# Performance work log

Measured on AMD Instinct MI355X. Metric: run time of the kernel, lower is better.

The kernel has to match this reference:

```python
import jax, jax.numpy as jnp
import numpy as np

HEAD_SIZE = 64
EMB_SIZE = 1024
B, N = 4, 4096


def setup_inputs() -> dict:
    key = jax.random.key(0)
    kx, kk, kq, kv = jax.random.split(key, 4)
    x = jax.random.normal(kx, (B, N, EMB_SIZE), dtype=jnp.float32)
    # nn.Linear(emb, head, bias=False): weight [head, emb]; y = x @ W.T
    s = 1.0 / np.sqrt(EMB_SIZE)
    Wk = jax.random.uniform(kk, (HEAD_SIZE, EMB_SIZE), jnp.float32, -s, s)
    Wq = jax.random.uniform(kq, (HEAD_SIZE, EMB_SIZE), jnp.float32, -s, s)
    Wv = jax.random.uniform(kv, (HEAD_SIZE, EMB_SIZE), jnp.float32, -s, s)
    return {"x": x, "Wk": Wk, "Wq": Wq, "Wv": Wv}


def reference(x, Wk, Wq, Wv):
    # k, q, v: [B, N, H]
    k = jnp.einsum("bne,he->bnh", x, Wk)
    q = jnp.einsum("bne,he->bnh", x, Wq)
    v = jnp.einsum("bne,he->bnh", x, Wv)
    scale = HEAD_SIZE ** -0.5
    aff = jnp.einsum("bqh,bkh->bqk", q, k) * scale  # [B, N, N]
    aff = jax.nn.softmax(aff, axis=2)
    # dropout rate is 0.0 -> identity
    return jnp.einsum("bqk,bkh->bqh", aff, v)
```

## Files before the change

kernel.cpp:

```cpp
#include <hip/hip_runtime.h>

#define NB   4
#define SEQ  4096
#define EMB  1024
#define HS   64

typedef __attribute__((ext_vector_type(8))) short bf16x8;
typedef __attribute__((ext_vector_type(4))) float f32x4;

__device__ inline unsigned short f2bf(float f) {
  unsigned int u = __float_as_uint(f);
  u += 0x7fffu + ((u >> 16) & 1u);
  return (unsigned short)(u >> 16);
}
__device__ inline float bf2f(unsigned short h) {
  return __uint_as_float(((unsigned int)h) << 16);
}
__device__ inline int swzi64(int row, int c) {
  return row * 64 + ((c ^ (row & 7)) << 3);
}
__device__ inline int swzi32(int row, int c) {
  return row * 32 + ((c ^ ((row >> 1) & 3)) << 3);
}
__device__ inline int swzi128(int row, int c) {
  return row * 128 + ((c ^ (row & 7)) << 3);
}
__device__ inline void gld16(const unsigned short* g, unsigned short* l) {
  __builtin_amdgcn_global_load_lds(
      (const __attribute__((address_space(1))) void*)g,
      (__attribute__((address_space(3))) void*)l, 16, 0, 0);
}

__global__ __launch_bounds__(256) void wprep(
    const float* __restrict__ Wk, const float* __restrict__ Wq,
    const float* __restrict__ Wv,
    unsigned short* __restrict__ Wh, unsigned short* __restrict__ Wl) {
  int i = blockIdx.x * 256 + threadIdx.x;
  int e = i >> 8, c = i & 255;
  float4 v;
  float sc = 1.0f;
  if (e < 64)       { v = ((const float4*)Wq)[e * 256 + c];
                      sc = 0.18033688011112042f; }
  else if (e < 128)   v = ((const float4*)Wk)[(e - 64) * 256 + c];
  else                v = ((const float4*)Wv)[(e - 128) * 256 + c];
  v.x *= sc; v.y *= sc; v.z *= sc; v.w *= sc;
  ushort4 hv, lv;
  hv.x = f2bf(v.x); lv.x = f2bf(v.x - bf2f(hv.x));
  hv.y = f2bf(v.y); lv.y = f2bf(v.y - bf2f(hv.y));
  hv.z = f2bf(v.z); lv.z = f2bf(v.z - bf2f(hv.z));
  hv.w = f2bf(v.w); lv.w = f2bf(v.w - bf2f(hv.w));
  *(ushort4*)&Wh[i * 4] = hv;
  *(ushort4*)&Wl[i * 4] = lv;
}

#define XhSp(p) ((unsigned short*)(SM + (p) * 2048))
#define XlSp(p) ((unsigned short*)(SM + 4096 + (p) * 2048))
#define WhSp(p) ((unsigned short*)(SM + 8192 + (p) * 12288))
#define WlSp(p) ((unsigned short*)(SM + 32768 + (p) * 12288))

__global__ __launch_bounds__(256) void qkv_x1(
    const float* __restrict__ x,
    const unsigned short* __restrict__ Wh, const unsigned short* __restrict__ Wl,
    unsigned short* __restrict__ qh, unsigned short* __restrict__ ql,
    unsigned short* __restrict__ kh, unsigned short* __restrict__ kl,
    unsigned short* __restrict__ vt) {
  __shared__ __align__(16) unsigned char SM[57344];

  const int t  = threadIdx.x;
  const int l  = t & 63;
  const int li = l & 15;
  const int g  = l >> 4;
  const int w  = t >> 6;
  const int m0 = blockIdx.x * 32;
  const int b  = m0 >> 12;
  const int n0 = m0 & 4095;

  const int xrow = t >> 3;
  const float* xp = x + (m0 + xrow) * EMB + (t & 7) * 4;
  const int xaddr = xrow * 32 + ((((t & 7) >> 1) ^ ((xrow >> 1) & 3)) << 3)
                    + (t & 1) * 4;

  const int wconst = (l >> 2) * EMB + (((l & 3) ^ ((l >> 3) & 3)) << 3);

  f32x4 acc[2][3];
#pragma unroll
  for (int i = 0; i < 2; ++i)
#pragma unroll
    for (int j = 0; j < 3; ++j) acc[i][j] = (f32x4){0.f, 0.f, 0.f, 0.f};

  const int rA0 = li, rA1 = 16 + li;
  const int rB0 = 48 * w + li, rB1 = rB0 + 16, rB2 = rB0 + 32;

  auto issueW = [&](int s, int p) {
    const int ko = s * 32;
#pragma unroll
    for (int i = 0; i < 3; ++i) {
      const int seg = 3 * w + i;
      gld16(Wh + 16 * seg * EMB + wconst + ko, WhSp(p) + seg * 512);
      gld16(Wl + 16 * seg * EMB + wconst + ko, WlSp(p) + seg * 512);
    }
  };
  auto writeX = [&](float4 v, int p) {
    unsigned short h0 = f2bf(v.x), h1 = f2bf(v.y), h2 = f2bf(v.z), h3 = f2bf(v.w);
    unsigned short e0 = f2bf(v.x - bf2f(h0)), e1 = f2bf(v.y - bf2f(h1));
    unsigned short e2 = f2bf(v.z - bf2f(h2)), e3 = f2bf(v.w - bf2f(h3));
    int2 hv, lv;
    hv.x = (int)((unsigned)h0 | ((unsigned)h1 << 16));
    hv.y = (int)((unsigned)h2 | ((unsigned)h3 << 16));
    lv.x = (int)((unsigned)e0 | ((unsigned)e1 << 16));
    lv.y = (int)((unsigned)e2 | ((unsigned)e3 << 16));
    *(int2*)&XhSp(p)[xaddr] = hv;
    *(int2*)&XlSp(p)[xaddr] = lv;
  };

  float4 px = *(const float4*)xp;
  issueW(0, 0);
  writeX(px, 0);
  px = *(const float4*)(xp + 32);
  __syncthreads();

  for (int s = 0; s < 32; ++s) {
    const int p = s & 1;
    if (s < 31) {
      issueW(s + 1, p ^ 1);
      writeX(px, p ^ 1);
      if (s < 30) px = *(const float4*)(xp + (s + 2) * 32);
    } else {
      asm volatile("s_waitcnt vmcnt(0)" ::: "memory");
    }
    __builtin_amdgcn_sched_barrier(0);

    bf16x8 ah0 = *(const bf16x8*)&XhSp(p)[swzi32(rA0, g)];
    bf16x8 ah1 = *(const bf16x8*)&XhSp(p)[swzi32(rA1, g)];
    bf16x8 al0 = *(const bf16x8*)&XlSp(p)[swzi32(rA0, g)];
    bf16x8 al1 = *(const bf16x8*)&XlSp(p)[swzi32(rA1, g)];
    bf16x8 bh0 = *(const bf16x8*)&WhSp(p)[swzi32(rB0, g)];
    bf16x8 bh1 = *(const bf16x8*)&WhSp(p)[swzi32(rB1, g)];
    bf16x8 bh2 = *(const bf16x8*)&WhSp(p)[swzi32(rB2, g)];
    bf16x8 bl0 = *(const bf16x8*)&WlSp(p)[swzi32(rB0, g)];
    bf16x8 bl1 = *(const bf16x8*)&WlSp(p)[swzi32(rB1, g)];
    bf16x8 bl2 = *(const bf16x8*)&WlSp(p)[swzi32(rB2, g)];

    __builtin_amdgcn_s_setprio(1);
    acc[0][0] = __builtin_amdgcn_mfma_f32_16x16x32_bf16(ah0, bh0, acc[0][0], 0,0,0);
    acc[0][0] = __builtin_amdgcn_mfma_f32_16x16x32_bf16(ah0, bl0, acc[0][0], 0,0,0);
    acc[0][0] = __builtin_amdgcn_mfma_f32_16x16x32_bf16(al0, bh0, acc[0][0], 0,0,0);
    acc[0][1] = __builtin_amdgcn_mfma_f32_16x16x32_bf16(ah0, bh1, acc[0][1], 0,0,0);
    acc[0][1] = __builtin_amdgcn_mfma_f32_16x16x32_bf16(ah0, bl1, acc[0][1], 0,0,0);
    acc[0][1] = __builtin_amdgcn_mfma_f32_16x16x32_bf16(al0, bh1, acc[0][1], 0,0,0);
    acc[0][2] = __builtin_amdgcn_mfma_f32_16x16x32_bf16(ah0, bh2, acc[0][2], 0,0,0);
    acc[0][2] = __builtin_amdgcn_mfma_f32_16x16x32_bf16(ah0, bl2, acc[0][2], 0,0,0);
    acc[0][2] = __builtin_amdgcn_mfma_f32_16x16x32_bf16(al0, bh2, acc[0][2], 0,0,0);
    acc[1][0] = __builtin_amdgcn_mfma_f32_16x16x32_bf16(ah1, bh0, acc[1][0], 0,0,0);
    acc[1][0] = __builtin_amdgcn_mfma_f32_16x16x32_bf16(ah1, bl0, acc[1][0], 0,0,0);
    acc[1][0] = __builtin_amdgcn_mfma_f32_16x16x32_bf16(al1, bh0, acc[1][0], 0,0,0);
    acc[1][1] = __builtin_amdgcn_mfma_f32_16x16x32_bf16(ah1, bh1, acc[1][1], 0,0,0);
    acc[1][1] = __builtin_amdgcn_mfma_f32_16x16x32_bf16(ah1, bl1, acc[1][1], 0,0,0);
    acc[1][1] = __builtin_amdgcn_mfma_f32_16x16x32_bf16(al1, bh1, acc[1][1], 0,0,0);
    acc[1][2] = __builtin_amdgcn_mfma_f32_16x16x32_bf16(ah1, bh2, acc[1][2], 0,0,0);
    acc[1][2] = __builtin_amdgcn_mfma_f32_16x16x32_bf16(ah1, bl2, acc[1][2], 0,0,0);
    acc[1][2] = __builtin_amdgcn_mfma_f32_16x16x32_bf16(al1, bh2, acc[1][2], 0,0,0);
    __builtin_amdgcn_s_setprio(0);

    asm volatile("s_waitcnt lgkmcnt(0)" ::: "memory");
    __builtin_amdgcn_s_barrier();
    __builtin_amdgcn_sched_barrier(0);
  }

#pragma unroll
  for (int i = 0; i < 2; ++i)
#pragma unroll
    for (int j = 0; j < 3; ++j) {
      const int H3 = 48 * w + 16 * j + li;
#pragma unroll
      for (int r = 0; r < 4; ++r) {
        const int mrow = 16 * i + 4 * g + r;
        const float vv = acc[i][j][r];
        if (H3 < 64) {
          const unsigned short hb = f2bf(vv);
          const int off = (b * SEQ + n0 + mrow) * HS + H3;
          qh[off] = hb; ql[off] = f2bf(vv - bf2f(hb));
        } else if (H3 < 128) {
          const unsigned short hb = f2bf(vv);
          const int off = (b * SEQ + n0 + mrow) * HS + (H3 - 64);
          kh[off] = hb; kl[off] = f2bf(vv - bf2f(hb));
        } else {
          vt[(b * HS + (H3 - 128)) * SEQ + n0 + mrow] = f2bf(vv);
        }
      }
    }
}

__global__ __launch_bounds__(512) void attn_mfma(
    const unsigned short* __restrict__ qh, const unsigned short* __restrict__ ql,
    const unsigned short* __restrict__ kh, const unsigned short* __restrict__ kl,
    const unsigned short* __restrict__ vt, float* __restrict__ out) {
  __shared__ __align__(16) unsigned char SM[155648];
  unsigned short* const PtS = (unsigned short*)(SM + 114688);

  const int t  = threadIdx.x;
  const int l  = t & 63;
  const int li = l & 15;
  const int g  = l >> 4;
  const int w  = t >> 6;
  const int qg = w & 1;
  const int ks = w >> 1;
  const int b  = blockIdx.y;
  const int q0 = blockIdx.x << 6;

  bf16x8 qfh[2][2], qfl[2][2];
#pragma unroll
  for (int qs = 0; qs < 2; ++qs) {
    const unsigned short* qrh = qh + (b * SEQ + q0 + 32 * qg + 16 * qs + li) * HS;
    const unsigned short* qrl = ql + (b * SEQ + q0 + 32 * qg + 16 * qs + li) * HS;
    qfh[qs][0] = *(const bf16x8*)&qrh[8 * g];
    qfh[qs][1] = *(const bf16x8*)&qrh[32 + 8 * g];
    qfl[qs][0] = *(const bf16x8*)&qrl[8 * g];
    qfl[qs][1] = *(const bf16x8*)&qrl[32 + 8 * g];
  }

  const int kconst = (l >> 3) * HS + (((l & 7) ^ (l >> 3)) << 3);
  const int rowl = l >> 4, slot = l & 15;
  const int vcE = rowl * SEQ + ((slot ^ rowl) << 3);
  const int vcO = rowl * SEQ + ((slot ^ (4 + rowl)) << 3);
  const unsigned short* khB = kh + b * SEQ * HS;
  const unsigned short* klB = kl + b * SEQ * HS;
  const unsigned short* vtB = vt + b * HS * SEQ;
  const int sA = 2 * w, sB = 2 * w + 1;

  f32x4 O[4][2];
#pragma unroll
  for (int ht = 0; ht < 4; ++ht) {
    O[ht][0] = (f32x4){0.f, 0.f, 0.f, 0.f};
    O[ht][1] = (f32x4){0.f, 0.f, 0.f, 0.f};
  }
  float lp0 = 0.f, lp1 = 0.f;

  auto stage = [&](int it, int pK, int vb) {
    const int kt0 = it << 7;
    unsigned short* const KhP = (unsigned short*)(SM + pK * 16384);
    unsigned short* const KlP = (unsigned short*)(SM + 32768 + pK * 16384);
    unsigned short* const VtP = (unsigned short*)(SM + 65536 + vb * 16384);
    gld16(khB + (kt0 + 8 * sA) * HS + kconst, KhP + sA * 512);
    gld16(khB + (kt0 + 8 * sB) * HS + kconst, KhP + sB * 512);
    gld16(klB + (kt0 + 8 * sA) * HS + kconst, KlP + sA * 512);
    gld16(klB + (kt0 + 8 * sB) * HS + kconst, KlP + sB * 512);
    gld16(vtB + 4 * sA * SEQ + kt0 + vcE, VtP + sA * 512);
    gld16(vtB + 4 * sB * SEQ + kt0 + vcO, VtP + sB * 512);
  };

  auto PV = [&](int slab, int vb) {
    unsigned short* const PtP = PtS + w * 2560 + slab * 1280;
    unsigned short* const VtP = (unsigned short*)(SM + 65536 + vb * 16384);
    bf16x8 pb0 = *(const bf16x8*)&PtP[li * 40 + ((g ^ (li & 3)) << 3)];
    const int r1 = 16 + li;
    bf16x8 pb1 = *(const bf16x8*)&PtP[r1 * 40 + ((g ^ (r1 & 3)) << 3)];
    __builtin_amdgcn_s_setprio(1);
#pragma unroll
    for (int ht = 0; ht < 4; ++ht) {
      const int vrow = 16 * ht + li;
      bf16x8 va = *(const bf16x8*)&VtP[swzi128(vrow, 4 * ks + g)];
      O[ht][0] = __builtin_amdgcn_mfma_f32_16x16x32_bf16(va, pb0, O[ht][0], 0,0,0);
      O[ht][1] = __builtin_amdgcn_mfma_f32_16x16x32_bf16(va, pb1, O[ht][1], 0,0,0);
    }
    __builtin_amdgcn_s_setprio(0);
  };

  stage(0, 0, 0);
  __syncthreads();

  int vbn = 1;
  int vbp = 2;
  for (int it = 0; it < 32; ++it) {
    const int p = it & 1;
    if (it < 31) stage(it + 1, p ^ 1, vbn);

    unsigned short* const KhS = (unsigned short*)(SM + p * 16384);
    unsigned short* const KlS = (unsigned short*)(SM + 32768 + p * 16384);

    f32x4 S[2][2];
    S[0][0] = (f32x4){-32.f, -32.f, -32.f, -32.f};
    S[0][1] = (f32x4){-32.f, -32.f, -32.f, -32.f};
    S[1][0] = (f32x4){-32.f, -32.f, -32.f, -32.f};
    S[1][1] = (f32x4){-32.f, -32.f, -32.f, -32.f};
    __builtin_amdgcn_s_setprio(1);
#pragma unroll
    for (int khf = 0; khf < 2; ++khf) {
      const int cc = 4 * khf + g;
#pragma unroll
      for (int kt = 0; kt < 2; ++kt) {
        const int row = 32 * ks + 16 * kt + li;
        bf16x8 akh = *(const bf16x8*)&KhS[swzi64(row, cc)];
        bf16x8 akl = *(const bf16x8*)&KlS[swzi64(row, cc)];
        S[kt][0] = __builtin_amdgcn_mfma_f32_16x16x32_bf16(akh, qfh[0][khf], S[kt][0], 0,0,0);
        S[kt][0] = __builtin_amdgcn_mfma_f32_16x16x32_bf16(akh, qfl[0][khf], S[kt][0], 0,0,0);
        S[kt][0] = __builtin_amdgcn_mfma_f32_16x16x32_bf16(akl, qfh[0][khf], S[kt][0], 0,0,0);
        S[kt][1] = __builtin_amdgcn_mfma_f32_16x16x32_bf16(akh, qfh[1][khf], S[kt][1], 0,0,0);
        S[kt][1] = __builtin_amdgcn_mfma_f32_16x16x32_bf16(akh, qfl[1][khf], S[kt][1], 0,0,0);
        S[kt][1] = __builtin_amdgcn_mfma_f32_16x16x32_bf16(akl, qfh[1][khf], S[kt][1], 0,0,0);
      }
    }
    __builtin_amdgcn_s_setprio(0);

    if (it > 0) PV(p ^ 1, vbp);

    unsigned short* const PtW = PtS + w * 2560 + p * 1280;
#pragma unroll
    for (int kt = 0; kt < 2; ++kt)
#pragma unroll
      for (int qs = 0; qs < 2; ++qs) {
        unsigned pu[4];
        float ls = 0.f;
#pragma unroll
        for (int r = 0; r < 4; ++r) {
          const float pe = exp2f(S[kt][qs][r]);
          pu[r] = __float_as_uint(pe);
          ls += __uint_as_float(pu[r] & 0xffff0000u);
        }
        if (qs == 0) lp0 += ls; else lp1 += ls;
        const unsigned p01 = __builtin_amdgcn_perm(pu[1], pu[0], 0x07060302u);
        const unsigned p23 = __builtin_amdgcn_perm(pu[3], pu[2], 0x07060302u);
        const int qrow = 16 * qs + li;
        const int c = 2 * kt + (g >> 1);
        const int addr = qrow * 40 + (((c ^ (qrow & 3))) << 3) + ((g & 1) << 2);
        int2 pv; pv.x = (int)p01; pv.y = (int)p23;
        *(int2*)&PtW[addr] = pv;
      }

    __syncthreads();

    vbn = (vbn == 2) ? 0 : vbn + 1;
    vbp = (vbp == 2) ? 0 : vbp + 1;
  }

  PV(1, 1);

  lp0 += __shfl_xor(lp0, 16); lp0 += __shfl_xor(lp0, 32);
  lp1 += __shfl_xor(lp1, 16); lp1 += __shfl_xor(lp1, 32);

  float* const OTm = (float*)SM;
  float* const Lm  = (float*)(SM + 65536);
#pragma unroll
  for (int ht = 0; ht < 4; ++ht)
#pragma unroll
    for (int qs = 0; qs < 2; ++qs) {
      float4 o4;
      o4.x = O[ht][qs][0]; o4.y = O[ht][qs][1];
      o4.z = O[ht][qs][2]; o4.w = O[ht][qs][3];
      *(float4*)&OTm[w * 2048 + (16 * qs + li) * 64 + 16 * ht + 4 * g] = o4;
    }
  if (g == 0) { Lm[w * 32 + li] = lp0; Lm[w * 32 + 16 + li] = lp1; }
  __syncthreads();

  {
    const int q = t >> 3, h8 = (t & 7) << 3;
    const int qq = q & 31, qgf = q >> 5;
    float lF = 0.f;
    float4 a = {0.f, 0.f, 0.f, 0.f}, c4 = {0.f, 0.f, 0.f, 0.f};
#pragma unroll
    for (int k2 = 0; k2 < 4; ++k2) {
      const int ww = qgf + 2 * k2;
      lF += Lm[ww * 32 + qq];
      const float* Ob = OTm + ww * 2048 + qq * 64 + h8;
      float4 u = *(const float4*)Ob;
      float4 v = *(const float4*)(Ob + 4);
      a.x += u.x; a.y += u.y; a.z += u.z; a.w += u.w;
      c4.x += v.x; c4.y += v.y; c4.z += v.z; c4.w += v.w;
    }
    const float inv = 1.f / lF;
    a.x *= inv; a.y *= inv; a.z *= inv; a.w *= inv;
    c4.x *= inv; c4.y *= inv; c4.z *= inv; c4.w *= inv;
    float* op = out + (b * SEQ + q0 + q) * HS + h8;
    *(float4*)op = a;
    *(float4*)(op + 4) = c4;
  }
}

extern "C" void kernel_launch(void* const* d_in, const int* in_sizes, int n_in,
                              void* d_out, int out_size, void* d_ws,
                              size_t ws_size, hipStream_t stream) {
  const float* x  = (const float*)d_in[0];
  const float* Wk = (const float*)d_in[1];
  const float* Wq = (const float*)d_in[2];
  const float* Wv = (const float*)d_in[3];
  float* out = (float*)d_out;

  unsigned short* us = (unsigned short*)d_ws;
  unsigned short* qh = us + 0 * (1 << 20);
  unsigned short* ql = us + 1 * (1 << 20);
  unsigned short* kh = us + 2 * (1 << 20);
  unsigned short* kl = us + 3 * (1 << 20);
  unsigned short* vt = us + 4 * (1 << 20);
  unsigned short* Wh = us + 5 * (1 << 20);
  unsigned short* Wl = Wh + 192 * 1024;

  wprep<<<192, 256, 0, stream>>>(Wk, Wq, Wv, Wh, Wl);
  qkv_x1<<<512, 256, 0, stream>>>(x, Wh, Wl, qh, ql, kh, kl, vt);
  attn_mfma<<<dim3(64, NB), 512, 0, stream>>>(qh, ql, kh, kl, vt, out);
}
```

Baseline: 183.8 us.

## Load K fragments directly into registers instead of staging through LDS

K hi/lo tiles are now read from global memory straight into per-wave register fragments, double-buffered across iterations, instead of being copied into shared memory and read back. Each wave now owns 16 keys and all 64 queries, so the QK^T split changes and P tiles are written into the slabs laid out for the PV stage. This drops LDS traffic for K and shrinks shared memory from about 152KB to 88KB, which may allow more resident blocks. The cost is more registers (Q fragments doubled, two K buffers) and exposed global-load latency on K.

```diff
diff --git a/kernel.cpp b/kernel.cpp
--- a/kernel.cpp
+++ b/kernel.cpp
@@ -15,9 +15,6 @@
 }
 __device__ inline float bf2f(unsigned short h) {
   return __uint_as_float(((unsigned int)h) << 16);
-}
-__device__ inline int swzi64(int row, int c) {
-  return row * 64 + ((c ^ (row & 7)) << 3);
 }
 __device__ inline int swzi32(int row, int c) {
   return row * 32 + ((c ^ ((row >> 1) & 3)) << 3);
@@ -195,36 +192,34 @@
     const unsigned short* __restrict__ qh, const unsigned short* __restrict__ ql,
     const unsigned short* __restrict__ kh, const unsigned short* __restrict__ kl,
     const unsigned short* __restrict__ vt, float* __restrict__ out) {
-  __shared__ __align__(16) unsigned char SM[155648];
-  unsigned short* const PtS = (unsigned short*)(SM + 114688);
+  __shared__ __align__(16) unsigned char SM[90112];
+  unsigned short* const PtS = (unsigned short*)(SM + 49152);
 
   const int t  = threadIdx.x;
   const int l  = t & 63;
   const int li = l & 15;
   const int g  = l >> 4;
   const int w  = t >> 6;
-  const int qg = w & 1;
-  const int ks = w >> 1;
   const int b  = blockIdx.y;
   const int q0 = blockIdx.x << 6;
 
-  bf16x8 qfh[2][2], qfl[2][2];
-#pragma unroll
-  for (int qs = 0; qs < 2; ++qs) {
-    const unsigned short* qrh = qh + (b * SEQ + q0 + 32 * qg + 16 * qs + li) * HS;
-    const unsigned short* qrl = ql + (b * SEQ + q0 + 32 * qg + 16 * qs + li) * HS;
+  bf16x8 qfh[4][2], qfl[4][2];
+#pragma unroll
+  for (int qs = 0; qs < 4; ++qs) {
+    const unsigned short* qrh = qh + (b * SEQ + q0 + 16 * qs + li) * HS;
+    const unsigned short* qrl = ql + (b * SEQ + q0 + 16 * qs + li) * HS;
     qfh[qs][0] = *(const bf16x8*)&qrh[8 * g];
     qfh[qs][1] = *(const bf16x8*)&qrh[32 + 8 * g];
     qfl[qs][0] = *(const bf16x8*)&qrl[8 * g];
     qfl[qs][1] = *(const bf16x8*)&qrl[32 + 8 * g];
   }
 
-  const int kconst = (l >> 3) * HS + (((l & 7) ^ (l >> 3)) << 3);
+  const unsigned short* const khR = kh + (b * SEQ + 16 * w + li) * HS + 8 * g;
+  const unsigned short* const klR = kl + (b * SEQ + 16 * w + li) * HS + 8 * g;
+
   const int rowl = l >> 4, slot = l & 15;
   const int vcE = rowl * SEQ + ((slot ^ rowl) << 3);
   const int vcO = rowl * SEQ + ((slot ^ (4 + rowl)) << 3);
-  const unsigned short* khB = kh + b * SEQ * HS;
-  const unsigned short* klB = kl + b * SEQ * HS;
   const unsigned short* vtB = vt + b * HS * SEQ;
   const int sA = 2 * w, sB = 2 * w + 1;
 
@@ -234,24 +229,29 @@
     O[ht][0] = (f32x4){0.f, 0.f, 0.f, 0.f};
     O[ht][1] = (f32x4){0.f, 0.f, 0.f, 0.f};
   }
-  float lp0 = 0.f, lp1 = 0.f;
-
-  auto stage = [&](int it, int pK, int vb) {
+  float lp[4] = {0.f, 0.f, 0.f, 0.f};
+
+  const int slabBase = (w & ~1);
+  const int cW = 2 * (w & 1) + (g >> 1);
+  const int subW = (g & 1) << 2;
+
+  auto stageV = [&](int it, int vb) {
     const int kt0 = it << 7;
-    unsigned short* const KhP = (unsigned short*)(SM + pK * 16384);
-    unsigned short* const KlP = (unsigned short*)(SM + 32768 + pK * 16384);
-    unsigned short* const VtP = (unsigned short*)(SM + 65536 + vb * 16384);
-    gld16(khB + (kt0 + 8 * sA) * HS + kconst, KhP + sA * 512);
-    gld16(khB + (kt0 + 8 * sB) * HS + kconst, KhP + sB * 512);
-    gld16(klB + (kt0 + 8 * sA) * HS + kconst, KlP + sA * 512);
-    gld16(klB + (kt0 + 8 * sB) * HS + kconst, KlP + sB * 512);
+    unsigned short* const VtP = (unsigned short*)(SM + vb * 16384);
     gld16(vtB + 4 * sA * SEQ + kt0 + vcE, VtP + sA * 512);
     gld16(vtB + 4 * sB * SEQ + kt0 + vcO, VtP + sB * 512);
   };
-
+  auto loadK = [&](int it, bf16x8 (&K)[4]) {
+    const int off = (it << 7) * HS;
+    K[0] = *(const bf16x8*)&khR[off];
+    K[1] = *(const bf16x8*)&khR[off + 32];
+    K[2] = *(const bf16x8*)&klR[off];
+    K[3] = *(const bf16x8*)&klR[off + 32];
+  };
   auto PV = [&](int slab, int vb) {
+    const int ks = w >> 1;
     unsigned short* const PtP = PtS + w * 2560 + slab * 1280;
-    unsigned short* const VtP = (unsigned short*)(SM + 65536 + vb * 16384);
+    unsigned short* const VtP = (unsigned short*)(SM + vb * 16384);
     bf16x8 pb0 = *(const bf16x8*)&PtP[li * 40 + ((g ^ (li & 3)) << 3)];
     const int r1 = 16 + li;
     bf16x8 pb1 = *(const bf16x8*)&PtP[r1 * 40 + ((g ^ (r1 & 3)) << 3)];
@@ -266,77 +266,77 @@
     __builtin_amdgcn_s_setprio(0);
   };
 
-  stage(0, 0, 0);
+  bf16x8 Ka[4], Kb[4];
+  loadK(0, Ka);
+  stageV(0, 0);
   __syncthreads();
 
   int vbn = 1;
   int vbp = 2;
-  for (int it = 0; it < 32; ++it) {
-    const int p = it & 1;
-    if (it < 31) stage(it + 1, p ^ 1, vbn);
-
-    unsigned short* const KhS = (unsigned short*)(SM + p * 16384);
-    unsigned short* const KlS = (unsigned short*)(SM + 32768 + p * 16384);
-
-    f32x4 S[2][2];
-    S[0][0] = (f32x4){-32.f, -32.f, -32.f, -32.f};
-    S[0][1] = (f32x4){-32.f, -32.f, -32.f, -32.f};
-    S[1][0] = (f32x4){-32.f, -32.f, -32.f, -32.f};
-    S[1][1] = (f32x4){-32.f, -32.f, -32.f, -32.f};
+
+  auto iter = [&](int it, int p, bf16x8 (&Kc)[4], bf16x8 (&Kn)[4]) {
+    if (it < 31) {
+      loadK(it + 1, Kn);
+      stageV(it + 1, vbn);
+    }
+
+    f32x4 S[4];
+#pragma unroll
+    for (int qs = 0; qs < 4; ++qs)
+      S[qs] = (f32x4){-32.f, -32.f, -32.f, -32.f};
     __builtin_amdgcn_s_setprio(1);
 #pragma unroll
     for (int khf = 0; khf < 2; ++khf) {
-      const int cc = 4 * khf + g;
-#pragma unroll
-      for (int kt = 0; kt < 2; ++kt) {
-        const int row = 32 * ks + 16 * kt + li;
-        bf16x8 akh = *(const bf16x8*)&KhS[swzi64(row, cc)];
-        bf16x8 akl = *(const bf16x8*)&KlS[swzi64(row, cc)];
-        S[kt][0] = __builtin_amdgcn_mfma_f32_16x16x32_bf16(akh, qfh[0][khf], S[kt][0], 0,0,0);
-        S[kt][0] = __builtin_amdgcn_mfma_f32_16x16x32_bf16(akh, qfl[0][khf], S[kt][0], 0,0,0);
-        S[kt][0] = __builtin_amdgcn_mfma_f32_16x16x32_bf16(akl, qfh[0][khf], S[kt][0], 0,0,0);
-        S[kt][1] = __builtin_amdgcn_mfma_f32_16x16x32_bf16(akh, qfh[1][khf], S[kt][1], 0,0,0);
-        S[kt][1] = __builtin_amdgcn_mfma_f32_16x16x32_bf16(akh, qfl[1][khf], S[kt][1], 0,0,0);
-        S[kt][1] = __builtin_amdgcn_mfma_f32_16x16x32_bf16(akl, qfh[1][khf], S[kt][1], 0,0,0);
+#pragma unroll
+      for (int qs = 0; qs < 4; ++qs) {
+        S[qs] = __builtin_amdgcn_mfma_f32_16x16x32_bf16(Kc[khf],     qfh[qs][khf], S[qs], 0,0,0);
+        S[qs] = __builtin_amdgcn_mfma_f32_16x16x32_bf16(Kc[khf],     qfl[qs][khf], S[qs], 0,0,0);
+        S[qs] = __builtin_amdgcn_mfma_f32_16x16x32_bf16(Kc[2 + khf], qfh[qs][khf], S[qs], 0,0,0);
       }
     }
     __builtin_amdgcn_s_setprio(0);
 
     if (it > 0) PV(p ^ 1, vbp);
 
-    unsigned short* const PtW = PtS + w * 2560 + p * 1280;
-#pragma unroll
-    for (int kt = 0; kt < 2; ++kt)
-#pragma unroll
-      for (int qs = 0; qs < 2; ++qs) {
-        unsigned pu[4];
-        float ls = 0.f;
-#pragma unroll
-        for (int r = 0; r < 4; ++r) {
-          const float pe = exp2f(S[kt][qs][r]);
-          pu[r] = __float_as_uint(pe);
-          ls += __uint_as_float(pu[r] & 0xffff0000u);
-        }
-        if (qs == 0) lp0 += ls; else lp1 += ls;
-        const unsigned p01 = __builtin_amdgcn_perm(pu[1], pu[0], 0x07060302u);
-        const unsigned p23 = __builtin_amdgcn_perm(pu[3], pu[2], 0x07060302u);
-        const int qrow = 16 * qs + li;
-        const int c = 2 * kt + (g >> 1);
-        const int addr = qrow * 40 + (((c ^ (qrow & 3))) << 3) + ((g & 1) << 2);
-        int2 pv; pv.x = (int)p01; pv.y = (int)p23;
-        *(int2*)&PtW[addr] = pv;
+#pragma unroll
+    for (int qs = 0; qs < 4; ++qs) {
+      unsigned pu[4];
+      float ls = 0.f;
+#pragma unroll
+      for (int r = 0; r < 4; ++r) {
+        const float pe = exp2f(S[qs][r]);
+        pu[r] = __float_as_uint(pe);
+        ls += __uint_as_float(pu[r] & 0xffff0000u);
       }
+      lp[qs] += ls;
+      const unsigned p01 = __builtin_amdgcn_perm(pu[1], pu[0], 0x07060302u);
+      const unsigned p23 = __builtin_amdgcn_perm(pu[3], pu[2], 0x07060302u);
+      const int slabIdx = slabBase + (qs >> 1);
+      const int qrow2 = 16 * (qs & 1) + li;
+      const int addr = qrow2 * 40 + (((cW ^ (qrow2 & 3))) << 3) + subW;
+      int2 pv; pv.x = (int)p01; pv.y = (int)p23;
+      *(int2*)&PtS[slabIdx * 2560 + p * 1280 + addr] = pv;
+    }
 
     __syncthreads();
 
     vbn = (vbn == 2) ? 0 : vbn + 1;
     vbp = (vbp == 2) ? 0 : vbp + 1;
+  };
+
+  for (int t2 = 0; t2 < 16; ++t2) {
+    iter(2 * t2,     0, Ka, Kb);
+    iter(2 * t2 + 1, 1, Kb, Ka);
   }
 
   PV(1, 1);
-
-  lp0 += __shfl_xor(lp0, 16); lp0 += __shfl_xor(lp0, 32);
-  lp1 += __shfl_xor(lp1, 16); lp1 += __shfl_xor(lp1, 32);
+  __syncthreads();
+
+#pragma unroll
+  for (int qs = 0; qs < 4; ++qs) {
+    lp[qs] += __shfl_xor(lp[qs], 16);
+    lp[qs] += __shfl_xor(lp[qs], 32);
+  }
 
   float* const OTm = (float*)SM;
   float* const Lm  = (float*)(SM + 65536);
@@ -349,18 +349,22 @@
       o4.z = O[ht][qs][2]; o4.w = O[ht][qs][3];
       *(float4*)&OTm[w * 2048 + (16 * qs + li) * 64 + 16 * ht + 4 * g] = o4;
     }
-  if (g == 0) { Lm[w * 32 + li] = lp0; Lm[w * 32 + 16 + li] = lp1; }
+  if (g == 0) {
+#pragma unroll
+    for (int qs = 0; qs < 4; ++qs) Lm[w * 64 + 16 * qs + li] = lp[qs];
+  }
   __syncthreads();
 
   {
     const int q = t >> 3, h8 = (t & 7) << 3;
     const int qq = q & 31, qgf = q >> 5;
     float lF = 0.f;
+#pragma unroll
+    for (int ww = 0; ww < 8; ++ww) lF += Lm[ww * 64 + q];
     float4 a = {0.f, 0.f, 0.f, 0.f}, c4 = {0.f, 0.f, 0.f, 0.f};
 #pragma unroll
     for (int k2 = 0; k2 < 4; ++k2) {
       const int ww = qgf + 2 * k2;
-      lF += Lm[ww * 32 + qq];
       const float* Ob = OTm + ww * 2048 + qq * 64 + h8;
       float4 u = *(const float4*)Ob;
       float4 v = *(const float4*)(Ob + 4);
```

Result: slower. 191.8 us (+4.4%).

## Split attention block across 16 waves instead of 8

Applied to the files above, without the earlier changes.

Doubles the attention block to 1024 threads (16 waves). Each wave now computes QK^T for a 16-key slice instead of 32 keys, and PV for half the head dimension, so per-wave work and registers halve. Staging loads are spread across twice as many waves. The aim is more latency hiding within the single resident block per CU, which the 155KB of shared memory forces. The cost is more waves contending at each barrier, more redundant Q-fragment loads, and a reshaped partial-sum reduction at the end.

```diff
diff --git a/kernel.cpp b/kernel.cpp
--- a/kernel.cpp
+++ b/kernel.cpp
@@ -191,7 +191,7 @@
     }
 }
 
-__global__ __launch_bounds__(512) void attn_mfma(
+__global__ __launch_bounds__(1024) void attn_mfma(
     const unsigned short* __restrict__ qh, const unsigned short* __restrict__ ql,
     const unsigned short* __restrict__ kh, const unsigned short* __restrict__ kl,
     const unsigned short* __restrict__ vt, float* __restrict__ out) {
@@ -204,7 +204,9 @@
   const int g  = l >> 4;
   const int w  = t >> 6;
   const int qg = w & 1;
-  const int ks = w >> 1;
+  const int kf = w >> 1;
+  const int ks2 = (w >> 1) & 3;
+  const int hh  = w >> 3;
   const int b  = blockIdx.y;
   const int q0 = blockIdx.x << 6;
 
@@ -221,47 +223,47 @@
 
   const int kconst = (l >> 3) * HS + (((l & 7) ^ (l >> 3)) << 3);
   const int rowl = l >> 4, slot = l & 15;
-  const int vcE = rowl * SEQ + ((slot ^ rowl) << 3);
-  const int vcO = rowl * SEQ + ((slot ^ (4 + rowl)) << 3);
+  const int vc = (w & 1) ? rowl * SEQ + ((slot ^ (4 + rowl)) << 3)
+                         : rowl * SEQ + ((slot ^ rowl) << 3);
   const unsigned short* khB = kh + b * SEQ * HS;
   const unsigned short* klB = kl + b * SEQ * HS;
   const unsigned short* vtB = vt + b * HS * SEQ;
-  const int sA = 2 * w, sB = 2 * w + 1;
-
-  f32x4 O[4][2];
-#pragma unroll
-  for (int ht = 0; ht < 4; ++ht) {
-    O[ht][0] = (f32x4){0.f, 0.f, 0.f, 0.f};
-    O[ht][1] = (f32x4){0.f, 0.f, 0.f, 0.f};
+
+  f32x4 O[2][2];
+#pragma unroll
+  for (int i = 0; i < 2; ++i) {
+    O[i][0] = (f32x4){0.f, 0.f, 0.f, 0.f};
+    O[i][1] = (f32x4){0.f, 0.f, 0.f, 0.f};
   }
   float lp0 = 0.f, lp1 = 0.f;
+
+  const int slabW = qg + 2 * (kf >> 1);
+  const int cW = 2 * (kf & 1) + (g >> 1);
+  const int subW = (g & 1) << 2;
 
   auto stage = [&](int it, int pK, int vb) {
     const int kt0 = it << 7;
     unsigned short* const KhP = (unsigned short*)(SM + pK * 16384);
     unsigned short* const KlP = (unsigned short*)(SM + 32768 + pK * 16384);
     unsigned short* const VtP = (unsigned short*)(SM + 65536 + vb * 16384);
-    gld16(khB + (kt0 + 8 * sA) * HS + kconst, KhP + sA * 512);
-    gld16(khB + (kt0 + 8 * sB) * HS + kconst, KhP + sB * 512);
-    gld16(klB + (kt0 + 8 * sA) * HS + kconst, KlP + sA * 512);
-    gld16(klB + (kt0 + 8 * sB) * HS + kconst, KlP + sB * 512);
-    gld16(vtB + 4 * sA * SEQ + kt0 + vcE, VtP + sA * 512);
-    gld16(vtB + 4 * sB * SEQ + kt0 + vcO, VtP + sB * 512);
+    gld16(khB + (kt0 + 8 * w) * HS + kconst, KhP + w * 512);
+    gld16(klB + (kt0 + 8 * w) * HS + kconst, KlP + w * 512);
+    gld16(vtB + 4 * w * SEQ + kt0 + vc, VtP + w * 512);
   };
 
-  auto PV = [&](int slab, int vb) {
-    unsigned short* const PtP = PtS + w * 2560 + slab * 1280;
+  auto PV = [&](int par, int vb) {
+    unsigned short* const PtP = PtS + (qg + 2 * ks2) * 2560 + par * 1280;
     unsigned short* const VtP = (unsigned short*)(SM + 65536 + vb * 16384);
     bf16x8 pb0 = *(const bf16x8*)&PtP[li * 40 + ((g ^ (li & 3)) << 3)];
     const int r1 = 16 + li;
     bf16x8 pb1 = *(const bf16x8*)&PtP[r1 * 40 + ((g ^ (r1 & 3)) << 3)];
     __builtin_amdgcn_s_setprio(1);
 #pragma unroll
-    for (int ht = 0; ht < 4; ++ht) {
-      const int vrow = 16 * ht + li;
-      bf16x8 va = *(const bf16x8*)&VtP[swzi128(vrow, 4 * ks + g)];
-      O[ht][0] = __builtin_amdgcn_mfma_f32_16x16x32_bf16(va, pb0, O[ht][0], 0,0,0);
-      O[ht][1] = __builtin_amdgcn_mfma_f32_16x16x32_bf16(va, pb1, O[ht][1], 0,0,0);
+    for (int ht2 = 0; ht2 < 2; ++ht2) {
+      const int vrow = 32 * hh + 16 * ht2 + li;
+      bf16x8 va = *(const bf16x8*)&VtP[swzi128(vrow, 4 * ks2 + g)];
+      O[ht2][0] = __builtin_amdgcn_mfma_f32_16x16x32_bf16(va, pb0, O[ht2][0], 0,0,0);
+      O[ht2][1] = __builtin_amdgcn_mfma_f32_16x16x32_bf16(va, pb1, O[ht2][1], 0,0,0);
     }
     __builtin_amdgcn_s_setprio(0);
   };
@@ -278,54 +280,44 @@
     unsigned short* const KhS = (unsigned short*)(SM + p * 16384);
     unsigned short* const KlS = (unsigned short*)(SM + 32768 + p * 16384);
 
-    f32x4 S[2][2];
-    S[0][0] = (f32x4){-32.f, -32.f, -32.f, -32.f};
-    S[0][1] = (f32x4){-32.f, -32.f, -32.f, -32.f};
-    S[1][0] = (f32x4){-32.f, -32.f, -32.f, -32.f};
-    S[1][1] = (f32x4){-32.f, -32.f, -32.f, -32.f};
+    f32x4 S[2];
+    S[0] = (f32x4){-32.f, -32.f, -32.f, -32.f};
+    S[1] = (f32x4){-32.f, -32.f, -32.f, -32.f};
     __builtin_amdgcn_s_setprio(1);
 #pragma unroll
     for (int khf = 0; khf < 2; ++khf) {
-      const int cc = 4 * khf + g;
-#pragma unroll
-      for (int kt = 0; kt < 2; ++kt) {
-        const int row = 32 * ks + 16 * kt + li;
-        bf16x8 akh = *(const bf16x8*)&KhS[swzi64(row, cc)];
-        bf16x8 akl = *(const bf16x8*)&KlS[swzi64(row, cc)];
-        S[kt][0] = __builtin_amdgcn_mfma_f32_16x16x32_bf16(akh, qfh[0][khf], S[kt][0], 0,0,0);
-        S[kt][0] = __builtin_amdgcn_mfma_f32_16x16x32_bf16(akh, qfl[0][khf], S[kt][0], 0,0,0);
-        S[kt][0] = __builtin_amdgcn_mfma_f32_16x16x32_bf16(akl, qfh[0][khf], S[kt][0], 0,0,0);
-        S[kt][1] = __builtin_amdgcn_mfma_f32_16x16x32_bf16(akh, qfh[1][khf], S[kt][1], 0,0,0);
-        S[kt][1] = __builtin_amdgcn_mfma_f32_16x16x32_bf16(akh, qfl[1][khf], S[kt][1], 0,0,0);
-        S[kt][1] = __builtin_amdgcn_mfma_f32_16x16x32_bf16(akl, qfh[1][khf], S[kt][1], 0,0,0);
+      const int row = 16 * kf + li;
+      bf16x8 akh = *(const bf16x8*)&KhS[swzi64(row, 4 * khf + g)];
+      bf16x8 akl = *(const bf16x8*)&KlS[swzi64(row, 4 * khf + g)];
+      S[0] = __builtin_amdgcn_mfma_f32_16x16x32_bf16(akh, qfh[0][khf], S[0], 0,0,0);
+      S[0] = __builtin_amdgcn_mfma_f32_16x16x32_bf16(akh, qfl[0][khf], S[0], 0,0,0);
+      S[0] = __builtin_amdgcn_mfma_f32_16x16x32_bf16(akl, qfh[0][khf], S[0], 0,0,0);
+      S[1] = __builtin_amdgcn_mfma_f32_16x16x32_bf16(akh, qfh[1][khf], S[1], 0,0,0);
+      S[1] = __builtin_amdgcn_mfma_f32_16x16x32_bf16(akh, qfl[1][khf], S[1], 0,0,0);
+      S[1] = __builtin_amdgcn_mfma_f32_16x16x32_bf16(akl, qfh[1][khf], S[1], 0,0,0);
+    }
+    __builtin_amdgcn_s_setprio(0);
+
+    if (it > 0) PV(p ^ 1, vbp);
+
+#pragma unroll
+    for (int qs = 0; qs < 2; ++qs) {
+      unsigned pu[4];
+      float ls = 0.f;
+#pragma unroll
+      for (int r = 0; r < 4; ++r) {
+        const float pe = exp2f(S[qs][r]);
+        pu[r] = __float_as_uint(pe);
+        ls += __uint_as_float(pu[r] & 0xffff0000u);
       }
-    }
-    __builtin_amdgcn_s_setprio(0);
-
-    if (it > 0) PV(p ^ 1, vbp);
-
-    unsigned short* const PtW = PtS + w * 2560 + p * 1280;
-#pragma unroll
-    for (int kt = 0; kt < 2; ++kt)
-#pragma unroll
-      for (int qs = 0; qs < 2; ++qs) {
-        unsigned pu[4];
-        float ls = 0.f;
-#pragma unroll
-        for (int r = 0; r < 4; ++r) {
-          const float pe = exp2f(S[kt][qs][r]);
-          pu[r] = __float_as_uint(pe);
-          ls += __uint_as_float(pu[r] & 0xffff0000u);
-        }
-        if (qs == 0) lp0 += ls; else lp1 += ls;
-        const unsigned p01 = __builtin_amdgcn_perm(pu[1], pu[0], 0x07060302u);
-        const unsigned p23 = __builtin_amdgcn_perm(pu[3], pu[2], 0x07060302u);
-        const int qrow = 16 * qs + li;
-        const int c = 2 * kt + (g >> 1);
-        const int addr = qrow * 40 + (((c ^ (qrow & 3))) << 3) + ((g & 1) << 2);
-        int2 pv; pv.x = (int)p01; pv.y = (int)p23;
-        *(int2*)&PtW[addr] = pv;
-      }
+      if (qs == 0) lp0 += ls; else lp1 += ls;
+      const unsigned p01 = __builtin_amdgcn_perm(pu[1], pu[0], 0x07060302u);
+      const unsigned p23 = __builtin_amdgcn_perm(pu[3], pu[2], 0x07060302u);
+      const int qrow = 16 * qs + li;
+      const int addr = qrow * 40 + (((cW ^ (qrow & 3))) << 3) + subW;
+      int2 pv; pv.x = (int)p01; pv.y = (int)p23;
+      *(int2*)&PtS[slabW * 2560 + p * 1280 + addr] = pv;
+    }
 
     __syncthreads();
 
@@ -341,38 +333,35 @@
   float* const OTm = (float*)SM;
   float* const Lm  = (float*)(SM + 65536);
 #pragma unroll
-  for (int ht = 0; ht < 4; ++ht)
+  for (int ht2 = 0; ht2 < 2; ++ht2)
 #pragma unroll
     for (int qs = 0; qs < 2; ++qs) {
       float4 o4;
-      o4.x = O[ht][qs][0]; o4.y = O[ht][qs][1];
-      o4.z = O[ht][qs][2]; o4.w = O[ht][qs][3];
-      *(float4*)&OTm[w * 2048 + (16 * qs + li) * 64 + 16 * ht + 4 * g] = o4;
+      o4.x = O[ht2][qs][0]; o4.y = O[ht2][qs][1];
+      o4.z = O[ht2][qs][2]; o4.w = O[ht2][qs][3];
+      *(float4*)&OTm[(((qg * 2 + hh) * 4 + ks2) << 10)
+                     + (16 * qs + li) * 32 + 16 * ht2 + 4 * g] = o4;
     }
   if (g == 0) { Lm[w * 32 + li] = lp0; Lm[w * 32 + 16 + li] = lp1; }
   __syncthreads();
 
   {
-    const int q = t >> 3, h8 = (t & 7) << 3;
+    const int q = t >> 4, hseg = (t & 15) << 2;
     const int qq = q & 31, qgf = q >> 5;
+    const int hhf = hseg >> 5, hsub = hseg & 31;
     float lF = 0.f;
-    float4 a = {0.f, 0.f, 0.f, 0.f}, c4 = {0.f, 0.f, 0.f, 0.f};
+#pragma unroll
+    for (int kff = 0; kff < 8; ++kff) lF += Lm[(qgf + 2 * kff) * 32 + qq];
+    float4 a = {0.f, 0.f, 0.f, 0.f};
 #pragma unroll
     for (int k2 = 0; k2 < 4; ++k2) {
-      const int ww = qgf + 2 * k2;
-      lF += Lm[ww * 32 + qq];
-      const float* Ob = OTm + ww * 2048 + qq * 64 + h8;
+      const float* Ob = OTm + (((qgf * 2 + hhf) * 4 + k2) << 10) + qq * 32 + hsub;
       float4 u = *(const float4*)Ob;
-      float4 v = *(const float4*)(Ob + 4);
       a.x += u.x; a.y += u.y; a.z += u.z; a.w += u.w;
-      c4.x += v.x; c4.y += v.y; c4.z += v.z; c4.w += v.w;
     }
     const float inv = 1.f / lF;
     a.x *= inv; a.y *= inv; a.z *= inv; a.w *= inv;
-    c4.x *= inv; c4.y *= inv; c4.z *= inv; c4.w *= inv;
-    float* op = out + (b * SEQ + q0 + q) * HS + h8;
-    *(float4*)op = a;
-    *(float4*)(op + 4) = c4;
+    *(float4*)(out + (b * SEQ + q0 + q) * HS + hseg) = a;
   }
 }
 
@@ -396,5 +385,5 @@
 
   wprep<<<192, 256, 0, stream>>>(Wk, Wq, Wv, Wh, Wl);
   qkv_x1<<<512, 256, 0, stream>>>(x, Wh, Wl, qh, ql, kh, kl, vt);
-  attn_mfma<<<dim3(64, NB), 512, 0, stream>>>(qh, ql, kh, kl, vt, out);
-}
+  attn_mfma<<<dim3(64, NB), 1024, 0, stream>>>(qh, ql, kh, kl, vt, out);
+}
```

Measured after the change: 177.6 us. -3.4%, faster.
